# Optimization experiments

Hardware: AMD Instinct MI355X
Metric: run time of the kernel (lower is better)

Reference implementation:

```python
import jax, jax.numpy as jnp
import numpy as np

N_STEPS = 6
LN_EPS = 1e-5

def _lin(x, w, b):
    # torch Linear: y = x @ W^T + b, w: [out, in]
    return jnp.matmul(x, w.T) + b

def _gelu(x):
    return jax.nn.gelu(x, approximate=False)

def setup_inputs() -> dict:
    key = jax.random.key(0)
    B, T, D, C, V, MS = 8, 1024, 512, 512, 32000, 1024
    ks = jax.random.split(key, 16)
    w = lambda k, shape: (jax.random.normal(k, shape, jnp.float32) * 0.02)
    return {
        "tokens": jax.random.randint(ks[0], (B, T), 0, V),
        "c_states": jax.random.normal(ks[1], (4, C), jnp.float32),
        "embed_w": w(ks[2], (V, D)),
        "pos_w": w(ks[3], (MS, D)),
        "cn_w1": w(ks[4], (2 * D, 4 * D)), "cn_b1": jnp.zeros((2 * D,), jnp.float32),
        "cn_w2": w(ks[5], (D, 2 * D)), "cn_b2": jnp.zeros((D,), jnp.float32),
        "ent_w1": w(ks[6], (64, D)), "ent_b1": jnp.zeros((64,), jnp.float32),
        "ent_w2": w(ks[7], (1, 64)), "ent_b2": jnp.zeros((1,), jnp.float32),
        "ctc_w1": w(ks[8], (2 * D, C)), "ctc_b1": jnp.zeros((2 * D,), jnp.float32),
        "ctc_w2": w(ks[9], (D, 2 * D)), "ctc_b2": jnp.zeros((D,), jnp.float32),
        "base_temp": jnp.asarray(2.0, jnp.float32),
        "ln_g": jnp.ones((D,), jnp.float32), "ln_b": jnp.zeros((D,), jnp.float32),
        "head_w": w(ks[10], (V, D)),
    }

def reference(tokens, c_states, embed_w, pos_w, cn_w1, cn_b1, cn_w2, cn_b2,
              ent_w1, ent_b1, ent_w2, ent_b2, ctc_w1, ctc_b1, ctc_w2, ctc_b2,
              base_temp, ln_g, ln_b, head_w):
    B, T = tokens.shape
    x = embed_w[tokens] + pos_w[:T][None, :, :]          # [B,T,D]
    c_pooled = c_states.mean(axis=0)                      # [C]
    c_constraint = _lin(_gelu(_lin(c_pooled, ctc_w1, ctc_b1)), ctc_w2, ctc_b2)  # [D]
    c_exp = jnp.broadcast_to(c_constraint, (B, T, c_constraint.shape[0]))
    sp_temp = jax.nn.softplus(base_temp)
    for step in range(N_STEPS):
        temp = sp_temp * (1.0 - step / N_STEPS * 0.8)
        left = jnp.roll(x, 1, axis=1)
        right = jnp.roll(x, -1, axis=1)
        ci = jnp.concatenate([x, left, right, c_exp], axis=-1)  # [B,T,4D]
        constraint = _lin(_gelu(_lin(ci, cn_w1, cn_b1)), cn_w2, cn_b2)  # [B,T,D]
        entropy = _lin(_gelu(_lin(x, ent_w1, ent_b1)), ent_w2, ent_b2)[..., 0]  # [B,T]
        cw = jax.nn.softmax(-entropy / temp, axis=-1)            # softmax over T
        x = x + constraint * cw[..., None] * 0.3
    mu = x.mean(axis=-1, keepdims=True)
    var = ((x - mu) ** 2).mean(axis=-1, keepdims=True)
    xn = (x - mu) * jax.lax.rsqrt(var + LN_EPS) * ln_g + ln_b
    return jnp.matmul(xn, head_w.T)                        # [B,T,V]
```

## Files before the change

kernel.cpp:

```cpp
#include <hip/hip_runtime.h>
#include <hip/hip_bf16.h>

typedef __hip_bfloat16 bf16_t;
typedef __bf16 bf16x8_t __attribute__((ext_vector_type(8)));
typedef float f32x4_t __attribute__((ext_vector_type(4)));

#define OFF_X     ((size_t)0)
#define OFF_XB    ((size_t)16777216)
#define OFF_H1    ((size_t)25165824)
#define OFF_XN    ((size_t)41943040)
#define OFF_HEADB ((size_t)50331648)
#define OFF_W1B   ((size_t)83099648)
#define OFF_W2B   ((size_t)86245376)
#define OFF_EW1   ((size_t)87293952)
#define OFF_ENT   ((size_t)87359488)
#define OFF_CW    ((size_t)87392256)
#define OFF_HC    ((size_t)87425024)
#define OFF_CC    ((size_t)87429120)
#define OFF_B1    ((size_t)87431168)

__device__ __forceinline__ float gelu_f(float v) {
    return 0.5f * v * (1.0f + erff(v * 0.7071067811865475f));
}

__device__ __forceinline__ void load_lds16(const bf16_t* g, bf16_t* l) {
    __builtin_amdgcn_global_load_lds(
        (const __attribute__((address_space(1))) void*)g,
        (__attribute__((address_space(3))) void*)l, 16, 0, 0);
}

__global__ void prep1_kernel(const float* __restrict__ cs, const float* __restrict__ w1,
                             const float* __restrict__ b1, float* __restrict__ hc) {
    int o = blockIdx.x * 256 + threadIdx.x;
    const float* wr = w1 + (size_t)o * 512;
    float acc = 0.f;
    for (int k = 0; k < 512; k += 4) {
        float4 w4 = *(const float4*)(wr + k);
        float4 a = *(const float4*)(cs + k);
        float4 b = *(const float4*)(cs + 512 + k);
        float4 c = *(const float4*)(cs + 1024 + k);
        float4 d = *(const float4*)(cs + 1536 + k);
        acc += w4.x * (a.x + b.x + c.x + d.x) * 0.25f;
        acc += w4.y * (a.y + b.y + c.y + d.y) * 0.25f;
        acc += w4.z * (a.z + b.z + c.z + d.z) * 0.25f;
        acc += w4.w * (a.w + b.w + c.w + d.w) * 0.25f;
    }
    hc[o] = gelu_f(acc + b1[o]);
}

__global__ void prep2_kernel(const float* __restrict__ hc, const float* __restrict__ w2,
                             const float* __restrict__ b2, float* __restrict__ cc) {
    int o = blockIdx.x * 256 + threadIdx.x;
    const float* wr = w2 + (size_t)o * 1024;
    float acc = 0.f;
    for (int k = 0; k < 1024; ++k) acc += wr[k] * hc[k];
    cc[o] = acc + b2[o];
}

__global__ void prep3_kernel(const float* __restrict__ cc, const float* __restrict__ cn_w1,
                             const float* __restrict__ cn_b1, float* __restrict__ bias1) {
    int o = blockIdx.x * 256 + threadIdx.x;
    const float* wr = cn_w1 + (size_t)o * 2048 + 1536;
    float acc = 0.f;
    for (int k = 0; k < 512; ++k) acc += wr[k] * cc[k];
    bias1[o] = acc + cn_b1[o];
}

__global__ void embed_kernel(const int* __restrict__ tokens, const float* __restrict__ ew,
                             const float* __restrict__ pw, float* __restrict__ x,
                             bf16_t* __restrict__ xb) {
    int idx = blockIdx.x * 256 + threadIdx.x;
    int d4 = idx & 127;
    int bt = idx >> 7;
    int t = bt & 1023;
    int tok = tokens[bt];
    float4 e = ((const float4*)(ew + (size_t)tok * 512))[d4];
    float4 p = ((const float4*)(pw + (size_t)t * 512))[d4];
    float4 o = make_float4(e.x + p.x, e.y + p.y, e.z + p.z, e.w + p.w);
    ((float4*)x)[idx] = o;
    __hip_bfloat162 p0, p1;
    p0.x = __float2bfloat16(o.x); p0.y = __float2bfloat16(o.y);
    p1.x = __float2bfloat16(o.z); p1.y = __float2bfloat16(o.w);
    ((__hip_bfloat162*)xb)[idx * 2]     = p0;
    ((__hip_bfloat162*)xb)[idx * 2 + 1] = p1;
}

__global__ void cvt_kernel(const float* __restrict__ src, bf16_t* __restrict__ dst) {
    int idx = blockIdx.x * 256 + threadIdx.x;
    float4 v = ((const float4*)src)[idx];
    __hip_bfloat162 p0, p1;
    p0.x = __float2bfloat16(v.x); p0.y = __float2bfloat16(v.y);
    p1.x = __float2bfloat16(v.z); p1.y = __float2bfloat16(v.w);
    ((__hip_bfloat162*)dst)[idx * 2]     = p0;
    ((__hip_bfloat162*)dst)[idx * 2 + 1] = p1;
}

__global__ void cvt_w1_kernel(const float* __restrict__ w1, bf16_t* __restrict__ dst) {
    int idx = blockIdx.x * 256 + threadIdx.x;
    int k4 = idx % 384;
    int o = idx / 384;
    float4 v = ((const float4*)(w1 + (size_t)o * 2048))[k4];
    __hip_bfloat162 p0, p1;
    p0.x = __float2bfloat16(v.x); p0.y = __float2bfloat16(v.y);
    p1.x = __float2bfloat16(v.z); p1.y = __float2bfloat16(v.w);
    ((__hip_bfloat162*)dst)[idx * 2]     = p0;
    ((__hip_bfloat162*)dst)[idx * 2 + 1] = p1;
}

__global__ __launch_bounds__(256) void entropy_mfma(
        const bf16_t* __restrict__ xb, const bf16_t* __restrict__ w1b,
        const float* __restrict__ b1, const float* __restrict__ w2,
        const float* __restrict__ b2, float* __restrict__ ent) {
    int wave = threadIdx.x >> 6, lane = threadIdx.x & 63;
    int lr = lane & 15, kq = lane >> 4;
    int tok0 = (blockIdx.x * 4 + wave) * 16;
    f32x4_t acc[4] = {};
    const bf16_t* xr = xb + (size_t)(tok0 + lr) * 512 + kq * 8;
    const bf16_t* wr = w1b + (size_t)lr * 512 + kq * 8;
    #pragma unroll 4
    for (int k0 = 0; k0 < 512; k0 += 32) {
        bf16x8_t a = *(const bf16x8_t*)(xr + k0);
        #pragma unroll
        for (int j = 0; j < 4; ++j) {
            bf16x8_t bb = *(const bf16x8_t*)(wr + (size_t)j * 16 * 512 + k0);
            acc[j] = __builtin_amdgcn_mfma_f32_16x16x32_bf16(a, bb, acc[j], 0, 0, 0);
        }
    }
    float p[4];
    #pragma unroll
    for (int r = 0; r < 4; ++r) {
        float s = 0.f;
        #pragma unroll
        for (int j = 0; j < 4; ++j) {
            int n = j * 16 + lr;
            s += gelu_f(acc[j][r] + b1[n]) * w2[n];
        }
        #pragma unroll
        for (int o = 1; o < 16; o <<= 1) s += __shfl_xor(s, o);
        p[r] = s;
    }
    if (lr == 0) {
        float bb = b2[0];
        #pragma unroll
        for (int r = 0; r < 4; ++r) ent[tok0 + kq * 4 + r] = p[r] + bb;
    }
}

__global__ void softmax_kernel(const float* __restrict__ ent, const float* __restrict__ btp,
                               float stepf, float* __restrict__ cw) {
    __shared__ float red[16];
    __shared__ float bc[2];
    int b = blockIdx.x, t = threadIdx.x;
    float bt = btp[0];
    float sp = (bt > 20.0f) ? bt : log1pf(expf(bt));
    float inv = -1.0f / (sp * stepf);
    float v = ent[b * 1024 + t] * inv;
    float m = v;
    #pragma unroll
    for (int o = 32; o; o >>= 1) m = fmaxf(m, __shfl_xor(m, o));
    if ((t & 63) == 0) red[t >> 6] = m;
    __syncthreads();
    if (t < 64) {
        float mm = (t < 16) ? red[t] : -3.4e38f;
        #pragma unroll
        for (int o = 32; o; o >>= 1) mm = fmaxf(mm, __shfl_xor(mm, o));
        if (t == 0) bc[0] = mm;
    }
    __syncthreads();
    float e = expf(v - bc[0]);
    float s = e;
    #pragma unroll
    for (int o = 32; o; o >>= 1) s += __shfl_xor(s, o);
    if ((t & 63) == 0) red[t >> 6] = s;
    __syncthreads();
    if (t < 64) {
        float ss = (t < 16) ? red[t] : 0.f;
        #pragma unroll
        for (int o = 32; o; o >>= 1) ss += __shfl_xor(ss, o);
        if (t == 0) bc[1] = ss;
    }
    __syncthreads();
    cw[b * 1024 + t] = e / bc[1];
}

__global__ void ln_kernel(const float* __restrict__ x, const float* __restrict__ g,
                          const float* __restrict__ b, bf16_t* __restrict__ xn) {
    int token = blockIdx.x * 4 + (threadIdx.x >> 6);
    int l = threadIdx.x & 63;
    const float* xr = x + (size_t)token * 512;
    float4 v0 = ((const float4*)xr)[l * 2];
    float4 v1 = ((const float4*)xr)[l * 2 + 1];
    float s = v0.x + v0.y + v0.z + v0.w + v1.x + v1.y + v1.z + v1.w;
    float ss = v0.x * v0.x + v0.y * v0.y + v0.z * v0.z + v0.w * v0.w
             + v1.x * v1.x + v1.y * v1.y + v1.z * v1.z + v1.w * v1.w;
    #pragma unroll
    for (int o = 32; o; o >>= 1) { s += __shfl_xor(s, o); ss += __shfl_xor(ss, o); }
    float mu = s * (1.0f / 512.0f);
    float var = ss * (1.0f / 512.0f) - mu * mu;
    float rs = rsqrtf(var + 1e-5f);
    float4 g0 = ((const float4*)g)[l * 2], g1 = ((const float4*)g)[l * 2 + 1];
    float4 b0 = ((const float4*)b)[l * 2], b1 = ((const float4*)b)[l * 2 + 1];
    bf16_t* op = xn + (size_t)token * 512 + l * 8;
    op[0] = __float2bfloat16((v0.x - mu) * rs * g0.x + b0.x);
    op[1] = __float2bfloat16((v0.y - mu) * rs * g0.y + b0.y);
    op[2] = __float2bfloat16((v0.z - mu) * rs * g0.z + b0.z);
    op[3] = __float2bfloat16((v0.w - mu) * rs * g0.w + b0.w);
    op[4] = __float2bfloat16((v1.x - mu) * rs * g1.x + b1.x);
    op[5] = __float2bfloat16((v1.y - mu) * rs * g1.y + b1.y);
    op[6] = __float2bfloat16((v1.z - mu) * rs * g1.z + b1.z);
    op[7] = __float2bfloat16((v1.w - mu) * rs * g1.w + b1.w);
}

template <int MODE, int ROLL>
__global__ __launch_bounds__(256) void gemm_bt(
    const bf16_t* __restrict__ A, int lda,
    const bf16_t* __restrict__ B, int ldb, int K,
    const float* __restrict__ bias,
    bf16_t* __restrict__ out_bf, int ldc,
    const float* __restrict__ cw, float* __restrict__ x)
{
    __shared__ __align__(16) bf16_t As[128 * 32];
    __shared__ __align__(16) bf16_t Bs[128 * 32];
    const int tid = threadIdx.x;
    const int m0 = blockIdx.x * 128;
    const int n0 = blockIdx.y * 128;
    const int wave = tid >> 6, lane = tid & 63;
    const int wm = (wave >> 1) * 64, wn = (wave & 1) * 64;
    const int lr = lane & 15, kq = lane >> 4;

    f32x4_t acc[4][4] = {};

    const int srow = tid >> 2;
    const int scol = (tid & 3) * 8;
    const bf16_t* gA = A + (size_t)(m0 + srow) * lda + scol;
    const bf16_t* gB = B + (size_t)(n0 + srow) * ldb + scol;
    bf16_t* lA = &As[srow * 32 + scol];
    bf16_t* lB = &Bs[srow * 32 + scol];
    const size_t a64 = (size_t)64 * lda, b64 = (size_t)64 * ldb;

    for (int k0 = 0; k0 < K; k0 += 32) {
        if (ROLL) {
            const int seg = k0 >> 9;
            const int kk = k0 & 511;
            const int sh = (seg == 0) ? 0 : ((seg == 1) ? 1023 : 1);
            const int r1 = m0 + srow;
            const int r2 = r1 + 64;
            const bf16_t* g1 = A + (size_t)((r1 & ~1023) | (((r1 & 1023) + sh) & 1023)) * 512 + kk + scol;
            const bf16_t* g2 = A + (size_t)((r2 & ~1023) | (((r2 & 1023) + sh) & 1023)) * 512 + kk + scol;
            load_lds16(g1, lA);
            load_lds16(g2, lA + 64 * 32);
        } else {
            load_lds16(gA + k0,       lA);
            load_lds16(gA + k0 + a64, lA + 64 * 32);
        }
        load_lds16(gB + k0,       lB);
        load_lds16(gB + k0 + b64, lB + 64 * 32);
        __syncthreads();
        bf16x8_t af[4], bfr[4];
        #pragma unroll
        for (int i = 0; i < 4; ++i) {
            af[i]  = *(const bf16x8_t*)&As[(wm + i * 16 + lr) * 32 + kq * 8];
            bfr[i] = *(const bf16x8_t*)&Bs[(wn + i * 16 + lr) * 32 + kq * 8];
        }
        #pragma unroll
        for (int i = 0; i < 4; ++i)
            #pragma unroll
            for (int j = 0; j < 4; ++j)
                acc[i][j] = __builtin_amdgcn_mfma_f32_16x16x32_bf16(af[i], bfr[j], acc[i][j], 0, 0, 0);
        __syncthreads();
    }

    #pragma unroll
    for (int i = 0; i < 4; ++i) {
        const int rbase = m0 + wm + i * 16 + kq * 4;
        #pragma unroll
        for (int j = 0; j < 4; ++j) {
            const int gcol = n0 + wn + j * 16 + lr;
            #pragma unroll
            for (int r = 0; r < 4; ++r) {
                const size_t grow = (size_t)(rbase + r);
                float v = acc[i][j][r];
                if (MODE == 0) {
                    v = gelu_f(v + bias[gcol]);
                    out_bf[grow * ldc + gcol] = __float2bfloat16(v);
                } else {
                    v += bias[gcol];
                    float nv = x[grow * ldc + gcol] + v * cw[grow] * 0.3f;
                    x[grow * ldc + gcol] = nv;
                    out_bf[grow * ldc + gcol] = __float2bfloat16(nv);
                }
            }
        }
    }
}

__global__ __launch_bounds__(512) void gemm_head(
    const bf16_t* __restrict__ A,
    const bf16_t* __restrict__ B,
    float* __restrict__ out)
{
    __shared__ __align__(16) bf16_t As[256 * 32];
    __shared__ __align__(16) bf16_t Bs[256 * 32];
    const int id = blockIdx.x + blockIdx.y * 32;
    const int nid = (id & 7) * 500 + (id >> 3);
    const int m0 = (nid & 31) * 256;
    const int n0 = (nid >> 5) * 256;

    const int tid = threadIdx.x;
    const int wave = tid >> 6, lane = tid & 63;
    const int wm = (wave >> 2) * 128, wn = (wave & 3) * 64;
    const int lr = lane & 15, kq = lane >> 4;

    f32x4_t acc[8][4] = {};

    const int srow = tid >> 2;
    const int scol = (tid & 3) * 8;
    const bf16_t* gA = A + (size_t)(m0 + srow) * 512 + scol;
    const bf16_t* gB = B + (size_t)(n0 + srow) * 512 + scol;
    bf16_t* lA = &As[srow * 32 + scol];
    bf16_t* lB = &Bs[srow * 32 + scol];
    const size_t s128 = (size_t)128 * 512;

    for (int k0 = 0; k0 < 512; k0 += 32) {
        load_lds16(gA + k0,        lA);
        load_lds16(gA + k0 + s128, lA + 128 * 32);
        load_lds16(gB + k0,        lB);
        load_lds16(gB + k0 + s128, lB + 128 * 32);
        __syncthreads();
        bf16x8_t af[8], bfr[4];
        #pragma unroll
        for (int i = 0; i < 8; ++i)
            af[i]  = *(const bf16x8_t*)&As[(wm + i * 16 + lr) * 32 + kq * 8];
        #pragma unroll
        for (int j = 0; j < 4; ++j)
            bfr[j] = *(const bf16x8_t*)&Bs[(wn + j * 16 + lr) * 32 + kq * 8];
        #pragma unroll
        for (int i = 0; i < 8; ++i)
            #pragma unroll
            for (int j = 0; j < 4; ++j)
                acc[i][j] = __builtin_amdgcn_mfma_f32_16x16x32_bf16(af[i], bfr[j], acc[i][j], 0, 0, 0);
        __syncthreads();
    }

    #pragma unroll
    for (int i = 0; i < 8; ++i) {
        const int rbase = m0 + wm + i * 16 + kq * 4;
        #pragma unroll
        for (int j = 0; j < 4; ++j) {
            const int gcol = n0 + wn + j * 16 + lr;
            #pragma unroll
            for (int r = 0; r < 4; ++r)
                out[(size_t)(rbase + r) * 32000 + gcol] = acc[i][j][r];
        }
    }
}

extern "C" void kernel_launch(void* const* d_in, const int* in_sizes, int n_in,
                              void* d_out, int out_size, void* d_ws, size_t ws_size,
                              hipStream_t stream) {
    const int*   tokens   = (const int*)d_in[0];
    const float* c_states = (const float*)d_in[1];
    const float* embed_w  = (const float*)d_in[2];
    const float* pos_w    = (const float*)d_in[3];
    const float* cn_w1    = (const float*)d_in[4];
    const float* cn_b1    = (const float*)d_in[5];
    const float* cn_b2    = (const float*)d_in[7];
    const float* cn_w2    = (const float*)d_in[6];
    const float* ent_w1   = (const float*)d_in[8];
    const float* ent_b1   = (const float*)d_in[9];
    const float* ent_w2   = (const float*)d_in[10];
    const float* ent_b2   = (const float*)d_in[11];
    const float* ctc_w1   = (const float*)d_in[12];
    const float* ctc_b1   = (const float*)d_in[13];
    const float* ctc_w2   = (const float*)d_in[14];
    const float* ctc_b2   = (const float*)d_in[15];
    const float* base_temp= (const float*)d_in[16];
    const float* ln_g     = (const float*)d_in[17];
    const float* ln_b     = (const float*)d_in[18];
    const float* head_w   = (const float*)d_in[19];
    float* out = (float*)d_out;

    char* ws = (char*)d_ws;
    float*  x     = (float*)(ws + OFF_X);
    bf16_t* xb    = (bf16_t*)(ws + OFF_XB);
    bf16_t* h1    = (bf16_t*)(ws + OFF_H1);
    bf16_t* xn    = (bf16_t*)(ws + OFF_XN);
    bf16_t* headb = (bf16_t*)(ws + OFF_HEADB);
    bf16_t* w1b   = (bf16_t*)(ws + OFF_W1B);
    bf16_t* w2b   = (bf16_t*)(ws + OFF_W2B);
    bf16_t* ew1b  = (bf16_t*)(ws + OFF_EW1);
    float*  ent   = (float*)(ws + OFF_ENT);
    float*  cw    = (float*)(ws + OFF_CW);
    float*  hc    = (float*)(ws + OFF_HC);
    float*  cc    = (float*)(ws + OFF_CC);
    float*  bias1 = (float*)(ws + OFF_B1);

    cvt_w1_kernel<<<1536, 256, 0, stream>>>(cn_w1, w1b);
    cvt_kernel<<<512, 256, 0, stream>>>(cn_w2, w2b);
    cvt_kernel<<<32, 256, 0, stream>>>(ent_w1, ew1b);
    prep1_kernel<<<4, 256, 0, stream>>>(c_states, ctc_w1, ctc_b1, hc);
    prep2_kernel<<<2, 256, 0, stream>>>(hc, ctc_w2, ctc_b2, cc);
    prep3_kernel<<<4, 256, 0, stream>>>(cc, cn_w1, cn_b1, bias1);
    embed_kernel<<<4096, 256, 0, stream>>>(tokens, embed_w, pos_w, x, xb);

    for (int step = 0; step < 6; ++step) {
        float stepf = 1.0f - ((float)step / 6.0f) * 0.8f;
        entropy_mfma<<<128, 256, 0, stream>>>(xb, ew1b, ent_b1, ent_w2, ent_b2, ent);
        softmax_kernel<<<8, 1024, 0, stream>>>(ent, base_temp, stepf, cw);
        gemm_bt<0, 1><<<dim3(64, 8), 256, 0, stream>>>(xb, 512, w1b, 1536, 1536,
                                                       bias1, h1, 1024, nullptr, nullptr);
        gemm_bt<1, 0><<<dim3(64, 4), 256, 0, stream>>>(h1, 1024, w2b, 1024, 1024,
                                                       cn_b2, xb, 512, cw, x);
    }

    cvt_kernel<<<16000, 256, 0, stream>>>(head_w, headb);
    ln_kernel<<<2048, 256, 0, stream>>>(x, ln_g, ln_b, xn);
    gemm_head<<<dim3(32, 125), 512, 0, stream>>>(xn, headb, out);
}
```

Measured before the change: 1.346 ms.

## Double-buffer LDS tiles in GEMM kernels to overlap global loads with MFMA

Both the step GEMM and the head GEMM now use two LDS buffers. The next K-slice is loaded directly into LDS while MFMAs run on the current slice, which replaces the two __syncthreads per iteration with one barrier after explicit waitcnt. The aim is to hide global-memory latency behind compute. In exchange LDS use per block doubles (64 KB for the head kernel), which may reduce occupancy.

Measured after the change: 1.299 ms. 3.5% less time.

```diff
diff --git a/kernel.cpp b/kernel.cpp
--- a/kernel.cpp
+++ b/kernel.cpp
@@ -219,8 +219,8 @@
     bf16_t* __restrict__ out_bf, int ldc,
     const float* __restrict__ cw, float* __restrict__ x)
 {
-    __shared__ __align__(16) bf16_t As[128 * 32];
-    __shared__ __align__(16) bf16_t Bs[128 * 32];
+    __shared__ __align__(16) bf16_t As[2 * 128 * 32];
+    __shared__ __align__(16) bf16_t Bs[2 * 128 * 32];
     const int tid = threadIdx.x;
     const int m0 = blockIdx.x * 128;
     const int n0 = blockIdx.y * 128;
@@ -234,11 +234,11 @@
     const int scol = (tid & 3) * 8;
     const bf16_t* gA = A + (size_t)(m0 + srow) * lda + scol;
     const bf16_t* gB = B + (size_t)(n0 + srow) * ldb + scol;
-    bf16_t* lA = &As[srow * 32 + scol];
-    bf16_t* lB = &Bs[srow * 32 + scol];
     const size_t a64 = (size_t)64 * lda, b64 = (size_t)64 * ldb;
 
-    for (int k0 = 0; k0 < K; k0 += 32) {
+    auto stage = [&](int k0, int c) {
+        bf16_t* lA = &As[c * 4096 + srow * 32 + scol];
+        bf16_t* lB = &Bs[c * 4096 + srow * 32 + scol];
         if (ROLL) {
             const int seg = k0 >> 9;
             const int kk = k0 & 511;
@@ -255,20 +255,40 @@
         }
         load_lds16(gB + k0,       lB);
         load_lds16(gB + k0 + b64, lB + 64 * 32);
-        __syncthreads();
+    };
+    auto compute = [&](int c) {
+        const bf16_t* cA = &As[c * 4096];
+        const bf16_t* cB = &Bs[c * 4096];
         bf16x8_t af[4], bfr[4];
         #pragma unroll
         for (int i = 0; i < 4; ++i) {
-            af[i]  = *(const bf16x8_t*)&As[(wm + i * 16 + lr) * 32 + kq * 8];
-            bfr[i] = *(const bf16x8_t*)&Bs[(wn + i * 16 + lr) * 32 + kq * 8];
+            af[i]  = *(const bf16x8_t*)&cA[(wm + i * 16 + lr) * 32 + kq * 8];
+            bfr[i] = *(const bf16x8_t*)&cB[(wn + i * 16 + lr) * 32 + kq * 8];
         }
         #pragma unroll
         for (int i = 0; i < 4; ++i)
             #pragma unroll
             for (int j = 0; j < 4; ++j)
                 acc[i][j] = __builtin_amdgcn_mfma_f32_16x16x32_bf16(af[i], bfr[j], acc[i][j], 0, 0, 0);
-        __syncthreads();
-    }
+    };
+
+    stage(0, 0);
+    asm volatile("s_waitcnt vmcnt(0)" ::: "memory");
+    __builtin_amdgcn_s_barrier();
+    __builtin_amdgcn_sched_barrier(0);
+
+    const int nt = K >> 5;
+    int cur = 0;
+    for (int t = 0; t < nt - 1; ++t) {
+        stage((t + 1) << 5, cur ^ 1);
+        compute(cur);
+        __builtin_amdgcn_sched_barrier(0);
+        asm volatile("s_waitcnt vmcnt(0) lgkmcnt(0)" ::: "memory");
+        __builtin_amdgcn_s_barrier();
+        __builtin_amdgcn_sched_barrier(0);
+        cur ^= 1;
+    }
+    compute(cur);
 
     #pragma unroll
     for (int i = 0; i < 4; ++i) {
@@ -299,8 +319,8 @@
     const bf16_t* __restrict__ B,
     float* __restrict__ out)
 {
-    __shared__ __align__(16) bf16_t As[256 * 32];
-    __shared__ __align__(16) bf16_t Bs[256 * 32];
+    __shared__ __align__(16) bf16_t As[2 * 256 * 32];
+    __shared__ __align__(16) bf16_t Bs[2 * 256 * 32];
     const int id = blockIdx.x + blockIdx.y * 32;
     const int nid = (id & 7) * 500 + (id >> 3);
     const int m0 = (nid & 31) * 256;
@@ -317,30 +337,49 @@
     const int scol = (tid & 3) * 8;
     const bf16_t* gA = A + (size_t)(m0 + srow) * 512 + scol;
     const bf16_t* gB = B + (size_t)(n0 + srow) * 512 + scol;
-    bf16_t* lA = &As[srow * 32 + scol];
-    bf16_t* lB = &Bs[srow * 32 + scol];
     const size_t s128 = (size_t)128 * 512;
 
-    for (int k0 = 0; k0 < 512; k0 += 32) {
+    auto stage = [&](int k0, int c) {
+        bf16_t* lA = &As[c * 8192 + srow * 32 + scol];
+        bf16_t* lB = &Bs[c * 8192 + srow * 32 + scol];
         load_lds16(gA + k0,        lA);
         load_lds16(gA + k0 + s128, lA + 128 * 32);
         load_lds16(gB + k0,        lB);
         load_lds16(gB + k0 + s128, lB + 128 * 32);
-        __syncthreads();
+    };
+    auto compute = [&](int c) {
+        const bf16_t* cA = &As[c * 8192];
+        const bf16_t* cB = &Bs[c * 8192];
         bf16x8_t af[8], bfr[4];
         #pragma unroll
         for (int i = 0; i < 8; ++i)
-            af[i]  = *(const bf16x8_t*)&As[(wm + i * 16 + lr) * 32 + kq * 8];
+            af[i]  = *(const bf16x8_t*)&cA[(wm + i * 16 + lr) * 32 + kq * 8];
         #pragma unroll
         for (int j = 0; j < 4; ++j)
-            bfr[j] = *(const bf16x8_t*)&Bs[(wn + j * 16 + lr) * 32 + kq * 8];
+            bfr[j] = *(const bf16x8_t*)&cB[(wn + j * 16 + lr) * 32 + kq * 8];
         #pragma unroll
         for (int i = 0; i < 8; ++i)
             #pragma unroll
             for (int j = 0; j < 4; ++j)
                 acc[i][j] = __builtin_amdgcn_mfma_f32_16x16x32_bf16(af[i], bfr[j], acc[i][j], 0, 0, 0);
-        __syncthreads();
-    }
+    };
+
+    stage(0, 0);
+    asm volatile("s_waitcnt vmcnt(0)" ::: "memory");
+    __builtin_amdgcn_s_barrier();
+    __builtin_amdgcn_sched_barrier(0);
+
+    int cur = 0;
+    for (int t = 0; t < 15; ++t) {
+        stage((t + 1) << 5, cur ^ 1);
+        compute(cur);
+        __builtin_amdgcn_sched_barrier(0);
+        asm volatile("s_waitcnt vmcnt(0) lgkmcnt(0)" ::: "memory");
+        __builtin_amdgcn_s_barrier();
+        __builtin_amdgcn_sched_barrier(0);
+        cur ^= 1;
+    }
+    compute(cur);
 
     #pragma unroll
     for (int i = 0; i < 8; ++i) {
@@ -364,8 +403,8 @@
     const float* pos_w    = (const float*)d_in[3];
     const float* cn_w1    = (const float*)d_in[4];
     const float* cn_b1    = (const float*)d_in[5];
+    const float* cn_w2    = (const float*)d_in[6];
     const float* cn_b2    = (const float*)d_in[7];
-    const float* cn_w2    = (const float*)d_in[6];
     const float* ent_w1   = (const float*)d_in[8];
     const float* ent_b1   = (const float*)d_in[9];
     const float* ent_w2   = (const float*)d_in[10];
```

## Unify GEMMs into double-buffered swizzled 8-wave pipelined kernel

Applied to the files above, without the earlier changes.

Replaces the single-buffered 128x128 GEMM and the separate head GEMM with one templated 256xBN kernel using 512 threads, BK=64, double-buffered LDS with an XOR swizzle, staged prefetch interleaved across sub-phases, and explicit vmcnt waits, barriers and setprio around the MFMA blocks. Block IDs are remapped for L2 locality. The goal is to hide global-load latency behind MFMA work and cut LDS bank conflicts and barrier overhead. In exchange it uses more LDS (about 96 KB for BN=256) and relies on hand-placed wait counts being exactly right.

Result: faster. 1.205 ms (-10.5%).

```diff
diff --git a/kernel.cpp b/kernel.cpp
--- a/kernel.cpp
+++ b/kernel.cpp
@@ -28,6 +28,13 @@
         (const __attribute__((address_space(1))) void*)g,
         (__attribute__((address_space(3))) void*)l, 16, 0, 0);
 }
+
+#define BAR()    __builtin_amdgcn_s_barrier()
+#define SCHED0() __builtin_amdgcn_sched_barrier(0)
+#define LGKM0()  asm volatile("s_waitcnt lgkmcnt(0)" ::: "memory")
+#define WAITV0() asm volatile("s_waitcnt vmcnt(0)" ::: "memory")
+#define WAITV2() asm volatile("s_waitcnt vmcnt(2)" ::: "memory")
+#define WAITV4() asm volatile("s_waitcnt vmcnt(4)" ::: "memory")
 
 __global__ void prep1_kernel(const float* __restrict__ cs, const float* __restrict__ w1,
                              const float* __restrict__ b1, float* __restrict__ hc) {
@@ -211,70 +218,140 @@
     op[7] = __float2bfloat16((v1.w - mu) * rs * g1.w + b1.w);
 }
 
-template <int MODE, int ROLL>
-__global__ __launch_bounds__(256) void gemm_bt(
+template <int MODE, int ROLL, int BN>
+__global__ __launch_bounds__(512, 2) void gemm8p(
     const bf16_t* __restrict__ A, int lda,
-    const bf16_t* __restrict__ B, int ldb, int K,
+    const bf16_t* __restrict__ B, int ldb, int K, int NMT,
     const float* __restrict__ bias,
     bf16_t* __restrict__ out_bf, int ldc,
-    const float* __restrict__ cw, float* __restrict__ x)
+    const float* __restrict__ cw, float* __restrict__ x,
+    float* __restrict__ out_f)
 {
-    __shared__ __align__(16) bf16_t As[128 * 32];
-    __shared__ __align__(16) bf16_t Bs[128 * 32];
+    constexpr int JJ = BN / 64;
+    __shared__ __align__(16) bf16_t As[2][256 * 64];
+    __shared__ __align__(16) bf16_t Bs[2][BN * 64];
+
+    const int NT = K >> 6;
+    const int nwg = gridDim.x;
+    const int id0 = blockIdx.x;
+    const int id = (id0 & 7) * (nwg >> 3) + (id0 >> 3);
+    const int m0 = (id % NMT) * 256;
+    const int n0 = (id / NMT) * BN;
+
     const int tid = threadIdx.x;
-    const int m0 = blockIdx.x * 128;
-    const int n0 = blockIdx.y * 128;
     const int wave = tid >> 6, lane = tid & 63;
-    const int wm = (wave >> 1) * 64, wn = (wave & 1) * 64;
+    const int wm = (wave >> 2) * 128;
+    const int wn = (wave & 3) * (BN / 4);
     const int lr = lane & 15, kq = lane >> 4;
 
-    f32x4_t acc[4][4] = {};
-
-    const int srow = tid >> 2;
-    const int scol = (tid & 3) * 8;
-    const bf16_t* gA = A + (size_t)(m0 + srow) * lda + scol;
-    const bf16_t* gB = B + (size_t)(n0 + srow) * ldb + scol;
-    bf16_t* lA = &As[srow * 32 + scol];
-    bf16_t* lB = &Bs[srow * 32 + scol];
-    const size_t a64 = (size_t)64 * lda, b64 = (size_t)64 * ldb;
-
-    for (int k0 = 0; k0 < K; k0 += 32) {
+    const int swz0 = (kq)     ^ (lr & 7);
+    const int swz1 = (4 + kq) ^ (lr & 7);
+    const int eoff0 = lr * 64 + swz0 * 8;
+    const int eoff1 = lr * 64 + swz1 * 8;
+
+    const int u0row = tid >> 3;
+    const int u1row = 64 + (tid >> 3);
+    const int usl   = tid & 7;
+    const int c0 = ((usl ^ (u0row & 7)) * 8);
+    const int c1 = ((usl ^ (u1row & 7)) * 8);
+
+    f32x4_t acc[8][JJ] = {};
+    bf16x8_t bfr[JJ][2];
+
+    auto stageA = [&](int ktile, int c, int half) {
+        const int kbase = ktile << 6;
+        const int r0 = m0 + half * 128 + u0row;
+        const int r1 = m0 + half * 128 + u1row;
+        const bf16_t *g0, *g1;
         if (ROLL) {
-            const int seg = k0 >> 9;
-            const int kk = k0 & 511;
+            const int seg = kbase >> 9;
+            const int kk2 = kbase & 511;
             const int sh = (seg == 0) ? 0 : ((seg == 1) ? 1023 : 1);
-            const int r1 = m0 + srow;
-            const int r2 = r1 + 64;
-            const bf16_t* g1 = A + (size_t)((r1 & ~1023) | (((r1 & 1023) + sh) & 1023)) * 512 + kk + scol;
-            const bf16_t* g2 = A + (size_t)((r2 & ~1023) | (((r2 & 1023) + sh) & 1023)) * 512 + kk + scol;
-            load_lds16(g1, lA);
-            load_lds16(g2, lA + 64 * 32);
+            const int s0 = (r0 & ~1023) | (((r0 & 1023) + sh) & 1023);
+            const int s1 = (r1 & ~1023) | (((r1 & 1023) + sh) & 1023);
+            g0 = A + (size_t)s0 * 512 + kk2 + c0;
+            g1 = A + (size_t)s1 * 512 + kk2 + c1;
         } else {
-            load_lds16(gA + k0,       lA);
-            load_lds16(gA + k0 + a64, lA + 64 * 32);
+            g0 = A + (size_t)r0 * lda + kbase + c0;
+            g1 = A + (size_t)r1 * lda + kbase + c1;
         }
-        load_lds16(gB + k0,       lB);
-        load_lds16(gB + k0 + b64, lB + 64 * 32);
-        __syncthreads();
-        bf16x8_t af[4], bfr[4];
-        #pragma unroll
-        for (int i = 0; i < 4; ++i) {
-            af[i]  = *(const bf16x8_t*)&As[(wm + i * 16 + lr) * 32 + kq * 8];
-            bfr[i] = *(const bf16x8_t*)&Bs[(wn + i * 16 + lr) * 32 + kq * 8];
+        bf16_t* l = &As[c][half * 128 * 64];
+        load_lds16(g0, l + tid * 8);
+        load_lds16(g1, l + (tid + 512) * 8);
+    };
+    auto stageB = [&](int ktile, int c, int half) {
+        const int kbase = ktile << 6;
+        const int r0 = n0 + half * 128 + u0row;
+        const int r1 = n0 + half * 128 + u1row;
+        const bf16_t* g0 = B + (size_t)r0 * ldb + kbase + c0;
+        const bf16_t* g1 = B + (size_t)r1 * ldb + kbase + c1;
+        bf16_t* l = &Bs[c][half * 128 * 64];
+        load_lds16(g0, l + tid * 8);
+        load_lds16(g1, l + (tid + 512) * 8);
+    };
+
+    stageA(0, 0, 0); stageA(0, 0, 1);
+    stageB(0, 0, 0); if (BN == 256) stageB(0, 0, 1);
+    stageB(1, 1, 0); if (BN == 256) stageB(1, 1, 1);
+    if (BN == 256) { WAITV4(); } else { WAITV2(); }
+    BAR();
+
+    int cur = 0;
+    for (int t = 0; t < NT; ++t) {
+        #pragma unroll
+        for (int p = 0; p < 4; ++p) {
+            bf16x8_t af0k0, af0k1, af1k0, af1k1;
+            {
+                const int r0 = (wm + 32 * p + lr) * 64;
+                const int r1 = (wm + 32 * p + 16 + lr) * 64;
+                af0k0 = *(const bf16x8_t*)&As[cur][r0 - lr * 64 + eoff0];
+                af0k1 = *(const bf16x8_t*)&As[cur][r0 - lr * 64 + eoff1];
+                af1k0 = *(const bf16x8_t*)&As[cur][r1 - lr * 64 + eoff0];
+                af1k1 = *(const bf16x8_t*)&As[cur][r1 - lr * 64 + eoff1];
+            }
+            if (p == 0) {
+                #pragma unroll
+                for (int j = 0; j < JJ; ++j) {
+                    const int rb = (wn + 16 * j) * 64;
+                    bfr[j][0] = *(const bf16x8_t*)&Bs[cur][rb + eoff0];
+                    bfr[j][1] = *(const bf16x8_t*)&Bs[cur][rb + eoff1];
+                }
+            }
+            if (p == 0 && t + 1 < NT) stageA(t + 1, cur ^ 1, 0);
+            if (p == 1 && t + 1 < NT) stageA(t + 1, cur ^ 1, 1);
+            if (p == 2 && t + 2 < NT) stageB(t + 2, cur, 0);
+            if (p == 3 && BN == 256 && t + 2 < NT) stageB(t + 2, cur, 1);
+
+            BAR();
+            LGKM0();
+            SCHED0();
+            __builtin_amdgcn_s_setprio(1);
+            #pragma unroll
+            for (int j = 0; j < JJ; ++j) {
+                acc[2*p][j]   = __builtin_amdgcn_mfma_f32_16x16x32_bf16(af0k0, bfr[j][0], acc[2*p][j],   0, 0, 0);
+                acc[2*p+1][j] = __builtin_amdgcn_mfma_f32_16x16x32_bf16(af1k0, bfr[j][0], acc[2*p+1][j], 0, 0, 0);
+            }
+            #pragma unroll
+            for (int j = 0; j < JJ; ++j) {
+                acc[2*p][j]   = __builtin_amdgcn_mfma_f32_16x16x32_bf16(af0k1, bfr[j][1], acc[2*p][j],   0, 0, 0);
+                acc[2*p+1][j] = __builtin_amdgcn_mfma_f32_16x16x32_bf16(af1k1, bfr[j][1], acc[2*p+1][j], 0, 0, 0);
+            }
+            __builtin_amdgcn_s_setprio(0);
+            SCHED0();
+            if (p == 3) {
+                if (t + 2 < NT) { if (BN == 256) { WAITV4(); } else { WAITV2(); } }
+                else           { WAITV0(); }
+            }
+            BAR();
         }
-        #pragma unroll
-        for (int i = 0; i < 4; ++i)
-            #pragma unroll
-            for (int j = 0; j < 4; ++j)
-                acc[i][j] = __builtin_amdgcn_mfma_f32_16x16x32_bf16(af[i], bfr[j], acc[i][j], 0, 0, 0);
-        __syncthreads();
+        cur ^= 1;
     }
 
     #pragma unroll
-    for (int i = 0; i < 4; ++i) {
+    for (int i = 0; i < 8; ++i) {
         const int rbase = m0 + wm + i * 16 + kq * 4;
         #pragma unroll
-        for (int j = 0; j < 4; ++j) {
+        for (int j = 0; j < JJ; ++j) {
             const int gcol = n0 + wn + j * 16 + lr;
             #pragma unroll
             for (int r = 0; r < 4; ++r) {
@@ -283,74 +360,15 @@
                 if (MODE == 0) {
                     v = gelu_f(v + bias[gcol]);
                     out_bf[grow * ldc + gcol] = __float2bfloat16(v);
-                } else {
+                } else if (MODE == 1) {
                     v += bias[gcol];
                     float nv = x[grow * ldc + gcol] + v * cw[grow] * 0.3f;
                     x[grow * ldc + gcol] = nv;
                     out_bf[grow * ldc + gcol] = __float2bfloat16(nv);
+                } else {
+                    out_f[grow * ldc + gcol] = v;
                 }
             }
-        }
-    }
-}
-
-__global__ __launch_bounds__(512) void gemm_head(
-    const bf16_t* __restrict__ A,
-    const bf16_t* __restrict__ B,
-    float* __restrict__ out)
-{
-    __shared__ __align__(16) bf16_t As[256 * 32];
-    __shared__ __align__(16) bf16_t Bs[256 * 32];
-    const int id = blockIdx.x + blockIdx.y * 32;
-    const int nid = (id & 7) * 500 + (id >> 3);
-    const int m0 = (nid & 31) * 256;
-    const int n0 = (nid >> 5) * 256;
-
-    const int tid = threadIdx.x;
-    const int wave = tid >> 6, lane = tid & 63;
-    const int wm = (wave >> 2) * 128, wn = (wave & 3) * 64;
-    const int lr = lane & 15, kq = lane >> 4;
-
-    f32x4_t acc[8][4] = {};
-
-    const int srow = tid >> 2;
-    const int scol = (tid & 3) * 8;
-    const bf16_t* gA = A + (size_t)(m0 + srow) * 512 + scol;
-    const bf16_t* gB = B + (size_t)(n0 + srow) * 512 + scol;
-    bf16_t* lA = &As[srow * 32 + scol];
-    bf16_t* lB = &Bs[srow * 32 + scol];
-    const size_t s128 = (size_t)128 * 512;
-
-    for (int k0 = 0; k0 < 512; k0 += 32) {
-        load_lds16(gA + k0,        lA);
-        load_lds16(gA + k0 + s128, lA + 128 * 32);
-        load_lds16(gB + k0,        lB);
-        load_lds16(gB + k0 + s128, lB + 128 * 32);
-        __syncthreads();
-        bf16x8_t af[8], bfr[4];
-        #pragma unroll
-        for (int i = 0; i < 8; ++i)
-            af[i]  = *(const bf16x8_t*)&As[(wm + i * 16 + lr) * 32 + kq * 8];
-        #pragma unroll
-        for (int j = 0; j < 4; ++j)
-            bfr[j] = *(const bf16x8_t*)&Bs[(wn + j * 16 + lr) * 32 + kq * 8];
-        #pragma unroll
-        for (int i = 0; i < 8; ++i)
-            #pragma unroll
-            for (int j = 0; j < 4; ++j)
-                acc[i][j] = __builtin_amdgcn_mfma_f32_16x16x32_bf16(af[i], bfr[j], acc[i][j], 0, 0, 0);
-        __syncthreads();
-    }
-
-    #pragma unroll
-    for (int i = 0; i < 8; ++i) {
-        const int rbase = m0 + wm + i * 16 + kq * 4;
-        #pragma unroll
-        for (int j = 0; j < 4; ++j) {
-            const int gcol = n0 + wn + j * 16 + lr;
-            #pragma unroll
-            for (int r = 0; r < 4; ++r)
-                out[(size_t)(rbase + r) * 32000 + gcol] = acc[i][j][r];
         }
     }
 }
@@ -364,8 +382,8 @@
     const float* pos_w    = (const float*)d_in[3];
     const float* cn_w1    = (const float*)d_in[4];
     const float* cn_b1    = (const float*)d_in[5];
+    const float* cn_w2    = (const float*)d_in[6];
     const float* cn_b2    = (const float*)d_in[7];
-    const float* cn_w2    = (const float*)d_in[6];
     const float* ent_w1   = (const float*)d_in[8];
     const float* ent_b1   = (const float*)d_in[9];
     const float* ent_w2   = (const float*)d_in[10];
@@ -407,13 +425,14 @@
         float stepf = 1.0f - ((float)step / 6.0f) * 0.8f;
         entropy_mfma<<<128, 256, 0, stream>>>(xb, ew1b, ent_b1, ent_w2, ent_b2, ent);
         softmax_kernel<<<8, 1024, 0, stream>>>(ent, base_temp, stepf, cw);
-        gemm_bt<0, 1><<<dim3(64, 8), 256, 0, stream>>>(xb, 512, w1b, 1536, 1536,
-                                                       bias1, h1, 1024, nullptr, nullptr);
-        gemm_bt<1, 0><<<dim3(64, 4), 256, 0, stream>>>(h1, 1024, w2b, 1024, 1024,
-                                                       cn_b2, xb, 512, cw, x);
+        gemm8p<0, 1, 128><<<256, 512, 0, stream>>>(xb, 512, w1b, 1536, 1536, 32,
+                                                   bias1, h1, 1024, nullptr, nullptr, nullptr);
+        gemm8p<1, 0, 128><<<128, 512, 0, stream>>>(h1, 1024, w2b, 1024, 1024, 32,
+                                                   cn_b2, xb, 512, cw, x, nullptr);
     }
 
     cvt_kernel<<<16000, 256, 0, stream>>>(head_w, headb);
     ln_kernel<<<2048, 256, 0, stream>>>(x, ln_g, ln_b, xn);
-    gemm_head<<<dim3(32, 125), 512, 0, stream>>>(xn, headb, out);
-}
+    gemm8p<2, 0, 256><<<4000, 512, 0, stream>>>(xn, 512, headb, 512, 512, 32,
+                                                nullptr, nullptr, 32000, nullptr, nullptr, out);
+}
```

## Double-buffer GEMMs with BK=64, swizzled LDS, XCD-aware remap, and fuse prep kernels

Applied to the files above, without the earlier changes.

Rewrites the step GEMMs and the head GEMM to use a BK=64 double-buffered LDS pipeline. Global-to-LDS loads for the next tiles are issued while MFMAs run on the current tile, with XOR-swizzled LDS layouts, explicit waitcnt/barrier placement and setprio around the MFMA blocks. The workgroup-id remap is extended to the step GEMMs so neighbouring tiles land on the same XCD. The three small constraint-prep kernels are fused into a single 1024-thread block that passes intermediates through shared memory. The aim is to hide memory latency and cut LDS bank conflicts, at the cost of doubled LDS use and hand-tuned vmcnt counts that are fragile.

After: 1.318 ms. -2.1%, faster.

```diff
diff --git a/kernel.cpp b/kernel.cpp
--- a/kernel.cpp
+++ b/kernel.cpp
@@ -15,9 +15,7 @@
 #define OFF_EW1   ((size_t)87293952)
 #define OFF_ENT   ((size_t)87359488)
 #define OFF_CW    ((size_t)87392256)
-#define OFF_HC    ((size_t)87425024)
-#define OFF_CC    ((size_t)87429120)
-#define OFF_B1    ((size_t)87431168)
+#define OFF_B1    ((size_t)87425024)
 
 __device__ __forceinline__ float gelu_f(float v) {
     return 0.5f * v * (1.0f + erff(v * 0.7071067811865475f));
@@ -29,41 +27,51 @@
         (__attribute__((address_space(3))) void*)l, 16, 0, 0);
 }
 
-__global__ void prep1_kernel(const float* __restrict__ cs, const float* __restrict__ w1,
-                             const float* __restrict__ b1, float* __restrict__ hc) {
-    int o = blockIdx.x * 256 + threadIdx.x;
-    const float* wr = w1 + (size_t)o * 512;
-    float acc = 0.f;
-    for (int k = 0; k < 512; k += 4) {
-        float4 w4 = *(const float4*)(wr + k);
-        float4 a = *(const float4*)(cs + k);
-        float4 b = *(const float4*)(cs + 512 + k);
-        float4 c = *(const float4*)(cs + 1024 + k);
-        float4 d = *(const float4*)(cs + 1536 + k);
-        acc += w4.x * (a.x + b.x + c.x + d.x) * 0.25f;
-        acc += w4.y * (a.y + b.y + c.y + d.y) * 0.25f;
-        acc += w4.z * (a.z + b.z + c.z + d.z) * 0.25f;
-        acc += w4.w * (a.w + b.w + c.w + d.w) * 0.25f;
-    }
-    hc[o] = gelu_f(acc + b1[o]);
-}
-
-__global__ void prep2_kernel(const float* __restrict__ hc, const float* __restrict__ w2,
-                             const float* __restrict__ b2, float* __restrict__ cc) {
-    int o = blockIdx.x * 256 + threadIdx.x;
-    const float* wr = w2 + (size_t)o * 1024;
-    float acc = 0.f;
-    for (int k = 0; k < 1024; ++k) acc += wr[k] * hc[k];
-    cc[o] = acc + b2[o];
-}
-
-__global__ void prep3_kernel(const float* __restrict__ cc, const float* __restrict__ cn_w1,
-                             const float* __restrict__ cn_b1, float* __restrict__ bias1) {
-    int o = blockIdx.x * 256 + threadIdx.x;
-    const float* wr = cn_w1 + (size_t)o * 2048 + 1536;
-    float acc = 0.f;
-    for (int k = 0; k < 512; ++k) acc += wr[k] * cc[k];
-    bias1[o] = acc + cn_b1[o];
+#define BAR()    __builtin_amdgcn_s_barrier()
+#define SCHED0() __builtin_amdgcn_sched_barrier(0)
+#define LGKM0()  asm volatile("s_waitcnt lgkmcnt(0)" ::: "memory")
+#define WAITV0() asm volatile("s_waitcnt vmcnt(0)" ::: "memory")
+#define WAITV4() asm volatile("s_waitcnt vmcnt(4)" ::: "memory")
+
+__global__ __launch_bounds__(1024) void prep_all(
+        const float* __restrict__ cs,
+        const float* __restrict__ ctc_w1, const float* __restrict__ ctc_b1,
+        const float* __restrict__ ctc_w2, const float* __restrict__ ctc_b2,
+        const float* __restrict__ cn_w1, const float* __restrict__ cn_b1,
+        float* __restrict__ bias1) {
+    __shared__ float hc_s[1024];
+    __shared__ float cc_s[512];
+    int o = threadIdx.x;
+    {
+        const float* wr = ctc_w1 + (size_t)o * 512;
+        float acc = 0.f;
+        for (int k = 0; k < 512; k += 4) {
+            float4 w4 = *(const float4*)(wr + k);
+            float4 a = *(const float4*)(cs + k);
+            float4 b = *(const float4*)(cs + 512 + k);
+            float4 c = *(const float4*)(cs + 1024 + k);
+            float4 d = *(const float4*)(cs + 1536 + k);
+            acc += w4.x * (a.x + b.x + c.x + d.x) * 0.25f;
+            acc += w4.y * (a.y + b.y + c.y + d.y) * 0.25f;
+            acc += w4.z * (a.z + b.z + c.z + d.z) * 0.25f;
+            acc += w4.w * (a.w + b.w + c.w + d.w) * 0.25f;
+        }
+        hc_s[o] = gelu_f(acc + ctc_b1[o]);
+    }
+    __syncthreads();
+    if (o < 512) {
+        const float* wr = ctc_w2 + (size_t)o * 1024;
+        float acc = 0.f;
+        for (int k = 0; k < 1024; ++k) acc += wr[k] * hc_s[k];
+        cc_s[o] = acc + ctc_b2[o];
+    }
+    __syncthreads();
+    {
+        const float* wr = cn_w1 + (size_t)o * 2048 + 1536;
+        float acc = 0.f;
+        for (int k = 0; k < 512; ++k) acc += wr[k] * cc_s[k];
+        bias1[o] = acc + cn_b1[o];
+    }
 }
 
 __global__ void embed_kernel(const int* __restrict__ tokens, const float* __restrict__ ew,
@@ -212,62 +220,107 @@
 }
 
 template <int MODE, int ROLL>
-__global__ __launch_bounds__(256) void gemm_bt(
+__global__ __launch_bounds__(256, 2) void gemm4p(
     const bf16_t* __restrict__ A, int lda,
-    const bf16_t* __restrict__ B, int ldb, int K,
+    const bf16_t* __restrict__ B, int ldb, int K, int NMT,
     const float* __restrict__ bias,
     bf16_t* __restrict__ out_bf, int ldc,
     const float* __restrict__ cw, float* __restrict__ x)
 {
-    __shared__ __align__(16) bf16_t As[128 * 32];
-    __shared__ __align__(16) bf16_t Bs[128 * 32];
+    __shared__ __align__(16) bf16_t As[2][128 * 64];
+    __shared__ __align__(16) bf16_t Bs[2][128 * 64];
+    const int NT = K >> 6;
+    const int nwg = gridDim.x;
+    const int id0 = blockIdx.x;
+    const int id = (id0 & 7) * (nwg >> 3) + (id0 >> 3);
+    const int m0 = (id % NMT) * 128;
+    const int n0 = (id / NMT) * 128;
+
     const int tid = threadIdx.x;
-    const int m0 = blockIdx.x * 128;
-    const int n0 = blockIdx.y * 128;
     const int wave = tid >> 6, lane = tid & 63;
     const int wm = (wave >> 1) * 64, wn = (wave & 1) * 64;
     const int lr = lane & 15, kq = lane >> 4;
 
+    const int eoff0 = lr * 64 + ((kq ^ (lr & 7)) * 8);
+    const int eoff1 = lr * 64 + (((4 + kq) ^ (lr & 7)) * 8);
+
+    const int trow = tid >> 3;
+    const int usl  = tid & 7;
+    const int sw8  = (usl ^ (trow & 7)) * 8;
+
     f32x4_t acc[4][4] = {};
 
-    const int srow = tid >> 2;
-    const int scol = (tid & 3) * 8;
-    const bf16_t* gA = A + (size_t)(m0 + srow) * lda + scol;
-    const bf16_t* gB = B + (size_t)(n0 + srow) * ldb + scol;
-    bf16_t* lA = &As[srow * 32 + scol];
-    bf16_t* lB = &Bs[srow * 32 + scol];
-    const size_t a64 = (size_t)64 * lda, b64 = (size_t)64 * ldb;
-
-    for (int k0 = 0; k0 < K; k0 += 32) {
-        if (ROLL) {
-            const int seg = k0 >> 9;
-            const int kk = k0 & 511;
-            const int sh = (seg == 0) ? 0 : ((seg == 1) ? 1023 : 1);
-            const int r1 = m0 + srow;
-            const int r2 = r1 + 64;
-            const bf16_t* g1 = A + (size_t)((r1 & ~1023) | (((r1 & 1023) + sh) & 1023)) * 512 + kk + scol;
-            const bf16_t* g2 = A + (size_t)((r2 & ~1023) | (((r2 & 1023) + sh) & 1023)) * 512 + kk + scol;
-            load_lds16(g1, lA);
-            load_lds16(g2, lA + 64 * 32);
-        } else {
-            load_lds16(gA + k0,       lA);
-            load_lds16(gA + k0 + a64, lA + 64 * 32);
-        }
-        load_lds16(gB + k0,       lB);
-        load_lds16(gB + k0 + b64, lB + 64 * 32);
-        __syncthreads();
-        bf16x8_t af[4], bfr[4];
+    auto stageA = [&](int ktile, int c) {
+        const int kbase = ktile << 6;
+        #pragma unroll
+        for (int h = 0; h < 4; ++h) {
+            const int r = m0 + h * 32 + trow;
+            const bf16_t* g;
+            if (ROLL) {
+                const int seg = kbase >> 9;
+                const int kk2 = kbase & 511;
+                const int sh = (seg == 0) ? 0 : ((seg == 1) ? 1023 : 1);
+                const int s = (r & ~1023) | (((r & 1023) + sh) & 1023);
+                g = A + (size_t)s * 512 + kk2 + sw8;
+            } else {
+                g = A + (size_t)r * lda + kbase + sw8;
+            }
+            load_lds16(g, &As[c][h * 32 * 64] + tid * 8);
+        }
+    };
+    auto stageB = [&](int ktile, int c) {
+        const int kbase = ktile << 6;
+        #pragma unroll
+        for (int h = 0; h < 4; ++h) {
+            const int r = n0 + h * 32 + trow;
+            load_lds16(B + (size_t)r * ldb + kbase + sw8, &Bs[c][h * 32 * 64] + tid * 8);
+        }
+    };
+
+    stageA(0, 0);
+    stageB(0, 0);
+    if (NT > 1) { stageB(1, 1); WAITV4(); } else { WAITV0(); }
+    BAR();
+    SCHED0();
+
+    int cur = 0;
+    for (int t = 0; t < NT; ++t) {
+        bf16x8_t af[4][2], bfj[4][2];
         #pragma unroll
         for (int i = 0; i < 4; ++i) {
-            af[i]  = *(const bf16x8_t*)&As[(wm + i * 16 + lr) * 32 + kq * 8];
-            bfr[i] = *(const bf16x8_t*)&Bs[(wn + i * 16 + lr) * 32 + kq * 8];
-        }
+            af[i][0] = *(const bf16x8_t*)&As[cur][(wm + i * 16) * 64 + eoff0];
+            af[i][1] = *(const bf16x8_t*)&As[cur][(wm + i * 16) * 64 + eoff1];
+        }
+        #pragma unroll
+        for (int j = 0; j < 4; ++j) {
+            bfj[j][0] = *(const bf16x8_t*)&Bs[cur][(wn + j * 16) * 64 + eoff0];
+            bfj[j][1] = *(const bf16x8_t*)&Bs[cur][(wn + j * 16) * 64 + eoff1];
+        }
+        if (t + 1 < NT) stageA(t + 1, cur ^ 1);
+        LGKM0();
+        SCHED0();
+        __builtin_amdgcn_s_setprio(1);
         #pragma unroll
         for (int i = 0; i < 4; ++i)
             #pragma unroll
             for (int j = 0; j < 4; ++j)
-                acc[i][j] = __builtin_amdgcn_mfma_f32_16x16x32_bf16(af[i], bfr[j], acc[i][j], 0, 0, 0);
-        __syncthreads();
+                acc[i][j] = __builtin_amdgcn_mfma_f32_16x16x32_bf16(af[i][0], bfj[j][0], acc[i][j], 0, 0, 0);
+        __builtin_amdgcn_s_setprio(0);
+        SCHED0();
+        BAR();
+        if (t + 2 < NT) stageB(t + 2, cur);
+        __builtin_amdgcn_s_setprio(1);
+        #pragma unroll
+        for (int i = 0; i < 4; ++i)
+            #pragma unroll
+            for (int j = 0; j < 4; ++j)
+                acc[i][j] = __builtin_amdgcn_mfma_f32_16x16x32_bf16(af[i][1], bfj[j][1], acc[i][j], 0, 0, 0);
+        __builtin_amdgcn_s_setprio(0);
+        SCHED0();
+        if (t + 2 < NT)      { WAITV4(); }
+        else if (t + 1 < NT) { WAITV0(); }
+        BAR();
+        cur ^= 1;
     }
 
     #pragma unroll
@@ -294,52 +347,96 @@
     }
 }
 
-__global__ __launch_bounds__(512) void gemm_head(
+__global__ __launch_bounds__(512, 2) void gemm_head(
     const bf16_t* __restrict__ A,
     const bf16_t* __restrict__ B,
     float* __restrict__ out)
 {
-    __shared__ __align__(16) bf16_t As[256 * 32];
-    __shared__ __align__(16) bf16_t Bs[256 * 32];
-    const int id = blockIdx.x + blockIdx.y * 32;
-    const int nid = (id & 7) * 500 + (id >> 3);
-    const int m0 = (nid & 31) * 256;
-    const int n0 = (nid >> 5) * 256;
+    __shared__ __align__(16) bf16_t As[2][256 * 64];
+    __shared__ __align__(16) bf16_t Bs[2][256 * 64];
+    const int id0 = blockIdx.x;
+    const int id = (id0 & 7) * 500 + (id0 >> 3);
+    const int m0 = (id % 32) * 256;
+    const int n0 = (id / 32) * 256;
 
     const int tid = threadIdx.x;
     const int wave = tid >> 6, lane = tid & 63;
     const int wm = (wave >> 2) * 128, wn = (wave & 3) * 64;
     const int lr = lane & 15, kq = lane >> 4;
 
+    const int eoff0 = lr * 64 + ((kq ^ (lr & 7)) * 8);
+    const int eoff1 = lr * 64 + (((4 + kq) ^ (lr & 7)) * 8);
+
+    const int trow = tid >> 3;
+    const int usl  = tid & 7;
+    const int sw8  = (usl ^ (trow & 7)) * 8;
+
     f32x4_t acc[8][4] = {};
-
-    const int srow = tid >> 2;
-    const int scol = (tid & 3) * 8;
-    const bf16_t* gA = A + (size_t)(m0 + srow) * 512 + scol;
-    const bf16_t* gB = B + (size_t)(n0 + srow) * 512 + scol;
-    bf16_t* lA = &As[srow * 32 + scol];
-    bf16_t* lB = &Bs[srow * 32 + scol];
-    const size_t s128 = (size_t)128 * 512;
-
-    for (int k0 = 0; k0 < 512; k0 += 32) {
-        load_lds16(gA + k0,        lA);
-        load_lds16(gA + k0 + s128, lA + 128 * 32);
-        load_lds16(gB + k0,        lB);
-        load_lds16(gB + k0 + s128, lB + 128 * 32);
-        __syncthreads();
-        bf16x8_t af[8], bfr[4];
-        #pragma unroll
-        for (int i = 0; i < 8; ++i)
-            af[i]  = *(const bf16x8_t*)&As[(wm + i * 16 + lr) * 32 + kq * 8];
-        #pragma unroll
-        for (int j = 0; j < 4; ++j)
-            bfr[j] = *(const bf16x8_t*)&Bs[(wn + j * 16 + lr) * 32 + kq * 8];
-        #pragma unroll
-        for (int i = 0; i < 8; ++i)
+    bf16x8_t bfr[4][2];
+
+    auto stageA = [&](int ktile, int c, int half) {
+        const int kbase = ktile << 6;
+        const bf16_t* g0 = A + (size_t)(m0 + half * 128 + trow) * 512 + kbase + sw8;
+        const bf16_t* g1 = A + (size_t)(m0 + half * 128 + 64 + trow) * 512 + kbase + sw8;
+        load_lds16(g0, &As[c][half * 8192] + tid * 8);
+        load_lds16(g1, &As[c][half * 8192 + 4096] + tid * 8);
+    };
+    auto stageB = [&](int ktile, int c, int half) {
+        const int kbase = ktile << 6;
+        const bf16_t* g0 = B + (size_t)(n0 + half * 128 + trow) * 512 + kbase + sw8;
+        const bf16_t* g1 = B + (size_t)(n0 + half * 128 + 64 + trow) * 512 + kbase + sw8;
+        load_lds16(g0, &Bs[c][half * 8192] + tid * 8);
+        load_lds16(g1, &Bs[c][half * 8192 + 4096] + tid * 8);
+    };
+
+    stageA(0, 0, 0); stageA(0, 0, 1);
+    stageB(0, 0, 0); stageB(0, 0, 1);
+    stageB(1, 1, 0); stageB(1, 1, 1);
+    WAITV4();
+    BAR();
+    SCHED0();
+
+    int cur = 0;
+    for (int t = 0; t < 8; ++t) {
+        #pragma unroll
+        for (int p = 0; p < 4; ++p) {
+            bf16x8_t a0k0 = *(const bf16x8_t*)&As[cur][(wm + 32 * p) * 64 + eoff0];
+            bf16x8_t a0k1 = *(const bf16x8_t*)&As[cur][(wm + 32 * p) * 64 + eoff1];
+            bf16x8_t a1k0 = *(const bf16x8_t*)&As[cur][(wm + 32 * p + 16) * 64 + eoff0];
+            bf16x8_t a1k1 = *(const bf16x8_t*)&As[cur][(wm + 32 * p + 16) * 64 + eoff1];
+            if (p == 0) {
+                #pragma unroll
+                for (int j = 0; j < 4; ++j) {
+                    bfr[j][0] = *(const bf16x8_t*)&Bs[cur][(wn + 16 * j) * 64 + eoff0];
+                    bfr[j][1] = *(const bf16x8_t*)&Bs[cur][(wn + 16 * j) * 64 + eoff1];
+                }
+            }
+            if (p == 0 && t + 1 < 8) stageA(t + 1, cur ^ 1, 0);
+            if (p == 1 && t + 1 < 8) stageA(t + 1, cur ^ 1, 1);
+            if (p == 2 && t + 2 < 8) stageB(t + 2, cur, 0);
+            if (p == 3 && t + 2 < 8) stageB(t + 2, cur, 1);
+            LGKM0();
+            SCHED0();
+            __builtin_amdgcn_s_setprio(1);
             #pragma unroll
-            for (int j = 0; j < 4; ++j)
-                acc[i][j] = __builtin_amdgcn_mfma_f32_16x16x32_bf16(af[i], bfr[j], acc[i][j], 0, 0, 0);
-        __syncthreads();
+            for (int j = 0; j < 4; ++j) {
+                acc[2*p][j]   = __builtin_amdgcn_mfma_f32_16x16x32_bf16(a0k0, bfr[j][0], acc[2*p][j],   0, 0, 0);
+                acc[2*p+1][j] = __builtin_amdgcn_mfma_f32_16x16x32_bf16(a1k0, bfr[j][0], acc[2*p+1][j], 0, 0, 0);
+            }
+            #pragma unroll
+            for (int j = 0; j < 4; ++j) {
+                acc[2*p][j]   = __builtin_amdgcn_mfma_f32_16x16x32_bf16(a0k1, bfr[j][1], acc[2*p][j],   0, 0, 0);
+                acc[2*p+1][j] = __builtin_amdgcn_mfma_f32_16x16x32_bf16(a1k1, bfr[j][1], acc[2*p+1][j], 0, 0, 0);
+            }
+            __builtin_amdgcn_s_setprio(0);
+            SCHED0();
+            if (p == 3) {
+                if (t + 2 < 8)      { WAITV4(); }
+                else if (t + 1 < 8) { WAITV0(); }
+            }
+            BAR();
+        }
+        cur ^= 1;
     }
 
     #pragma unroll
@@ -364,8 +461,8 @@
     const float* pos_w    = (const float*)d_in[3];
     const float* cn_w1    = (const float*)d_in[4];
     const float* cn_b1    = (const float*)d_in[5];
+    const float* cn_w2    = (const float*)d_in[6];
     const float* cn_b2    = (const float*)d_in[7];
-    const float* cn_w2    = (const float*)d_in[6];
     const float* ent_w1   = (const float*)d_in[8];
     const float* ent_b1   = (const float*)d_in[9];
     const float* ent_w2   = (const float*)d_in[10];
@@ -391,29 +488,26 @@
     bf16_t* ew1b  = (bf16_t*)(ws + OFF_EW1);
     float*  ent   = (float*)(ws + OFF_ENT);
     float*  cw    = (float*)(ws + OFF_CW);
-    float*  hc    = (float*)(ws + OFF_HC);
-    float*  cc    = (float*)(ws + OFF_CC);
     float*  bias1 = (float*)(ws + OFF_B1);
 
     cvt_w1_kernel<<<1536, 256, 0, stream>>>(cn_w1, w1b);
     cvt_kernel<<<512, 256, 0, stream>>>(cn_w2, w2b);
     cvt_kernel<<<32, 256, 0, stream>>>(ent_w1, ew1b);
-    prep1_kernel<<<4, 256, 0, stream>>>(c_states, ctc_w1, ctc_b1, hc);
-    prep2_kernel<<<2, 256, 0, stream>>>(hc, ctc_w2, ctc_b2, cc);
-    prep3_kernel<<<4, 256, 0, stream>>>(cc, cn_w1, cn_b1, bias1);
+    prep_all<<<1, 1024, 0, stream>>>(c_states, ctc_w1, ctc_b1, ctc_w2, ctc_b2,
+                                     cn_w1, cn_b1, bias1);
     embed_kernel<<<4096, 256, 0, stream>>>(tokens, embed_w, pos_w, x, xb);
 
     for (int step = 0; step < 6; ++step) {
         float stepf = 1.0f - ((float)step / 6.0f) * 0.8f;
         entropy_mfma<<<128, 256, 0, stream>>>(xb, ew1b, ent_b1, ent_w2, ent_b2, ent);
         softmax_kernel<<<8, 1024, 0, stream>>>(ent, base_temp, stepf, cw);
-        gemm_bt<0, 1><<<dim3(64, 8), 256, 0, stream>>>(xb, 512, w1b, 1536, 1536,
-                                                       bias1, h1, 1024, nullptr, nullptr);
-        gemm_bt<1, 0><<<dim3(64, 4), 256, 0, stream>>>(h1, 1024, w2b, 1024, 1024,
-                                                       cn_b2, xb, 512, cw, x);
+        gemm4p<0, 1><<<512, 256, 0, stream>>>(xb, 512, w1b, 1536, 1536, 64,
+                                              bias1, h1, 1024, nullptr, nullptr);
+        gemm4p<1, 0><<<256, 256, 0, stream>>>(h1, 1024, w2b, 1024, 1024, 64,
+                                              cn_b2, xb, 512, cw, x);
     }
 
     cvt_kernel<<<16000, 256, 0, stream>>>(head_w, headb);
     ln_kernel<<<2048, 256, 0, stream>>>(x, ln_g, ln_b, xn);
-    gemm_head<<<dim3(32, 125), 512, 0, stream>>>(xn, headb, out);
-}
+    gemm_head<<<4000, 512, 0, stream>>>(xn, headb, out);
+}
```
